# Kernel optimization log

Measured on AMD Instinct MI355X. Metric: run time of the kernel, lower is better.

Reference implementation:

```python
import jax, jax.numpy as jnp
import numpy as np

# Blade order: 1 | e0 e1 e2 e3 | e01 e02 e03 e12 e13 e23 | e012 e013 e023 e123 | e0123
GRADE = jnp.array([0, 1, 1, 1, 1, 2, 2, 2, 2, 2, 2, 3, 3, 3, 3, 4])
# Invariant bilinear form <~A B>_0 for signature (+,-,-,-)
METRIC = jnp.array([1., 1., -1., -1., -1., -1., -1., -1., 1., 1., 1., 1., 1., 1., -1., -1.], dtype=jnp.float32)
NUM_HEADS, HID_MV, HID_S = 8, 8, 32


def equi_linear(mv, s, w_mv, w_s2mv, w_mv2s, w_s, b_mv, b_s):
    """Pin(1,3)-equivariant linear layer: grade-projection basis maps + scalar<->grade-0 mixing."""
    w16 = w_mv[:, :, GRADE]  # (out_mv, in_mv, 16): one weight per grade, broadcast over blades
    out_mv = jnp.einsum('oix,...ix->...ox', w16, mv)
    out_mv = out_mv.at[..., 0].add(jnp.einsum('oi,...i->...o', w_s2mv, s) + b_mv)
    out_s = (jnp.einsum('oi,...i->...o', w_s, s)
             + jnp.einsum('oi,...i->...o', w_mv2s, mv[..., 0]) + b_s)
    return out_mv, out_s


def setup_inputs() -> dict:
    key = jax.random.key(0)
    ks = jax.random.split(key, 20)
    B, Nq, Nkv = 4, 2048, 2048
    H, Cm, Cs = NUM_HEADS, HID_MV, HID_S

    def w(k, shape, fan_in):
        return jax.random.normal(k, shape, jnp.float32) / np.sqrt(fan_in).astype(np.float32)

    return {
        'multivectors_kv': jax.random.normal(ks[0], (B, Nkv, 16, 16), jnp.float32),
        'multivectors_q': jax.random.normal(ks[1], (B, Nq, 16, 16), jnp.float32),
        'scalars_kv': jax.random.normal(ks[2], (B, Nkv, 64), jnp.float32),
        'scalars_q': jax.random.normal(ks[3], (B, Nq, 64), jnp.float32),
        # q_linear: 16 mv -> Cm*H=64 mv, 64 s -> Cs*H=256 s
        'wq_mv': w(ks[4], (Cm * H, 16, 5), 16), 'wq_s2mv': w(ks[5], (Cm * H, 64), 64),
        'wq_mv2s': w(ks[6], (Cs * H, 16), 16), 'wq_s': w(ks[7], (Cs * H, 64), 64),
        'bq_mv': jnp.zeros((Cm * H,), jnp.float32), 'bq_s': jnp.zeros((Cs * H,), jnp.float32),
        # kv_linear: 16 mv -> 2*Cm=16 mv, 64 s -> 2*Cs=64 s (multi-query: shared across heads)
        'wkv_mv': w(ks[8], (2 * Cm, 16, 5), 16), 'wkv_s2mv': w(ks[9], (2 * Cm, 64), 64),
        'wkv_mv2s': w(ks[10], (2 * Cs, 16), 16), 'wkv_s': w(ks[11], (2 * Cs, 64), 64),
        'bkv_mv': jnp.zeros((2 * Cm,), jnp.float32), 'bkv_s': jnp.zeros((2 * Cs,), jnp.float32),
        # out_linear: Cm*H=64 mv -> 16 mv, Cs*H=256 s -> 64 s
        'wo_mv': w(ks[12], (16, Cm * H, 5), Cm * H), 'wo_s2mv': w(ks[13], (16, Cs * H), Cs * H),
        'wo_mv2s': w(ks[14], (64, Cm * H), Cm * H), 'wo_s': w(ks[15], (64, Cs * H), Cs * H),
        'bo_mv': jnp.zeros((16,), jnp.float32), 'bo_s': jnp.zeros((64,), jnp.float32),
        'head_scale': jnp.ones((H,), jnp.float32),
    }


def reference(multivectors_kv, multivectors_q, scalars_kv, scalars_q,
              wq_mv, wq_s2mv, wq_mv2s, wq_s, bq_mv, bq_s,
              wkv_mv, wkv_s2mv, wkv_mv2s, wkv_s, bkv_mv, bkv_s,
              wo_mv, wo_s2mv, wo_mv2s, wo_s, bo_mv, bo_s, head_scale):
    B, Nq = multivectors_q.shape[0], multivectors_q.shape[1]
    H, Cm, Cs = NUM_HEADS, HID_MV, HID_S

    q_mv, q_s = equi_linear(multivectors_q, scalars_q, wq_mv, wq_s2mv, wq_mv2s, wq_s, bq_mv, bq_s)
    kv_mv, kv_s = equi_linear(multivectors_kv, scalars_kv, wkv_mv, wkv_s2mv, wkv_mv2s, wkv_s, bkv_mv, bkv_s)
    k_mv, v_mv = jnp.split(kv_mv, 2, axis=-2)  # (B,Nkv,Cm,16) each
    k_s, v_s = jnp.split(kv_s, 2, axis=-1)     # (B,Nkv,Cs) each

    # einops '(hidden num_heads)': hidden is the outer factor
    q_mv = jnp.moveaxis(q_mv.reshape(B, Nq, Cm, H, 16), 3, 1)  # (B,H,Nq,Cm,16)
    q_s = jnp.moveaxis(q_s.reshape(B, Nq, Cs, H), 3, 1)        # (B,H,Nq,Cs)

    scale = np.float32(1.0 / np.sqrt(16 * Cm + Cs))  # flattened feature dim
    scores = (jnp.einsum('bhqcx,bkcx->bhqk', q_mv, k_mv * METRIC)
              + jnp.einsum('bhqs,bks->bhqk', q_s, k_s)) * scale
    attn = jax.nn.softmax(scores, axis=-1)  # (B,H,Nq,Nkv)
    h_mv = jnp.einsum('bhqk,bkcx->bhqcx', attn, v_mv)
    h_s = jnp.einsum('bhqk,bks->bhqs', attn, v_s)

    h_mv = h_mv * head_scale[None, :, None, None, None]
    h_s = h_s * head_scale[None, :, None, None]

    # '(n_heads hidden_channels)': heads outer
    h_mv = jnp.moveaxis(h_mv, 1, 2).reshape(B, Nq, H * Cm, 16)
    h_s = jnp.moveaxis(h_s, 1, 2).reshape(B, Nq, H * Cs)

    return equi_linear(h_mv, h_s, wo_mv, wo_s2mv, wo_mv2s, wo_s, bo_mv, bo_s)
```

## Files before the change

### kernel.cpp

```cpp
#include <hip/hip_runtime.h>
#include <hip/hip_bf16.h>
#include <cstdint>

#define H_  8
#define B_  4
#define NQ  2048
#define NKV 2048
#define DF  160

typedef __attribute__((ext_vector_type(8))) short bf16x8;
typedef __attribute__((ext_vector_type(4))) float f32x4;

__constant__ int   c_grade[16]  = {0,1,1,1,1,2,2,2,2,2,2,3,3,3,3,4};
__constant__ float c_metric[16] = {1.f,1.f,-1.f,-1.f,-1.f,-1.f,-1.f,-1.f,
                                   1.f,1.f,1.f,1.f,1.f,1.f,-1.f,-1.f};

#define SCALE_LOG2E 0.11405506f

__device__ __forceinline__ unsigned short f2bf(float f) {
    union { float f; unsigned u; } v; v.f = f;
    return (unsigned short)((v.u + 0x7FFFu + ((v.u >> 16) & 1u)) >> 16);
}
__device__ __forceinline__ float bf2f(unsigned short u) {
    union { unsigned u; float f; } v; v.u = ((unsigned)u) << 16;
    return v.f;
}

__global__ __launch_bounds__(256) void qproj_kernel(
    const float* __restrict__ mvq,
    const float* __restrict__ sq,
    const float* __restrict__ w_mv,
    const float* __restrict__ w_s2mv,
    const float* __restrict__ w_mv2s,
    const float* __restrict__ w_s,
    const float* __restrict__ b_mv,
    const float* __restrict__ b_s,
    unsigned short* __restrict__ Qbuf)
{
    const int tok0 = blockIdx.x * 16;
    const int b = tok0 / NQ, n0 = tok0 % NQ;
    const int t = threadIdx.x;

    __shared__ float mv_t[256][20];
    __shared__ float s_t[64][20];
    __shared__ float smadd[64][20];

    #pragma unroll
    for (int k = 0; k < 16; ++k)
        mv_t[t][k] = mvq[(size_t)(tok0 + k) * 256 + t];
    {
        int e = t & 63, tb = t >> 6;
        #pragma unroll
        for (int k = 0; k < 4; ++k)
            s_t[e][tb + 4 * k] = sq[(size_t)(tok0 + tb + 4 * k) * 64 + e];
    }
    __syncthreads();

    {
        int o = t >> 2, tg = t & 3;
        f32x4 acc = {0.f, 0.f, 0.f, 0.f};
        for (int i = 0; i < 64; ++i)
            acc += w_s2mv[o * 64 + i] * *(const f32x4*)&s_t[i][tg * 4];
        acc += b_mv[o];
        *(f32x4*)&smadd[o][tg * 4] = acc;
    }
    __syncthreads();

    const int x = t & 15;
    const int g = c_grade[x];
    #pragma unroll
    for (int p = 0; p < 4; ++p) {
        int o = (t >> 4) + 16 * p;
        f32x4 acc[4] = {{0,0,0,0},{0,0,0,0},{0,0,0,0},{0,0,0,0}};
        #pragma unroll
        for (int i = 0; i < 16; ++i) {
            float w = w_mv[(o * 16 + i) * 5 + g];
            #pragma unroll
            for (int k = 0; k < 4; ++k)
                acc[k] += w * *(const f32x4*)&mv_t[i * 16 + x][k * 4];
        }
        if (x == 0) {
            #pragma unroll
            for (int k = 0; k < 4; ++k)
                acc[k] += *(const f32x4*)&smadd[o][k * 4];
        }
        int c = o >> 3, h = o & 7;
        #pragma unroll
        for (int k = 0; k < 4; ++k)
            #pragma unroll
            for (int j = 0; j < 4; ++j)
                Qbuf[((size_t)(b * H_ + h) * NQ + n0 + k * 4 + j) * DF + c * 16 + x] =
                    f2bf(acc[k][j] * SCALE_LOG2E);
    }

    {
        f32x4 acc[4] = {{0,0,0,0},{0,0,0,0},{0,0,0,0},{0,0,0,0}};
        const float4* ws4 = (const float4*)w_s;
        #pragma unroll
        for (int ii = 0; ii < 16; ++ii) {
            float4 w4 = ws4[t * 16 + ii];
            #pragma unroll
            for (int c = 0; c < 4; ++c) {
                float w = (&w4.x)[c];
                #pragma unroll
                for (int k = 0; k < 4; ++k)
                    acc[k] += w * *(const f32x4*)&s_t[ii * 4 + c][k * 4];
            }
        }
        #pragma unroll
        for (int i = 0; i < 16; ++i) {
            float w = w_mv2s[t * 16 + i];
            #pragma unroll
            for (int k = 0; k < 4; ++k)
                acc[k] += w * *(const f32x4*)&mv_t[i * 16][k * 4];
        }
        float bs = b_s[t];
        int cs = t >> 3, h = t & 7;
        #pragma unroll
        for (int k = 0; k < 4; ++k)
            #pragma unroll
            for (int j = 0; j < 4; ++j)
                Qbuf[((size_t)(b * H_ + h) * NQ + n0 + k * 4 + j) * DF + 128 + cs] =
                    f2bf((acc[k][j] + bs) * SCALE_LOG2E);
    }
}

__global__ __launch_bounds__(256) void kvproj_kernel(
    const float* __restrict__ mvkv, const float* __restrict__ skv,
    const float* __restrict__ w_mv,
    const float* __restrict__ w_s2mv,
    const float* __restrict__ w_mv2s,
    const float* __restrict__ w_s,
    const float* __restrict__ b_mv,
    const float* __restrict__ b_s,
    unsigned short* __restrict__ Kbuf,
    unsigned short* __restrict__ Vtbuf)
{
    const int tok0 = blockIdx.x * 16;
    const int b = tok0 / NKV, n0 = tok0 % NKV;
    const int t = threadIdx.x;

    __shared__ float mv_t[256][20];
    __shared__ float s_t[64][20];
    __shared__ float smadd[16][20];

    #pragma unroll
    for (int k = 0; k < 16; ++k)
        mv_t[t][k] = mvkv[(size_t)(tok0 + k) * 256 + t];
    {
        int e = t & 63, tb = t >> 6;
        #pragma unroll
        for (int k = 0; k < 4; ++k)
            s_t[e][tb + 4 * k] = skv[(size_t)(tok0 + tb + 4 * k) * 64 + e];
    }
    __syncthreads();

    {
        int o = t >> 4, tau = t & 15;
        float acc = 0.f;
        for (int i = 0; i < 64; ++i)
            acc += w_s2mv[o * 64 + i] * s_t[i][tau];
        smadd[o][tau] = acc + b_mv[o];
    }
    __syncthreads();

    {
        int o = t >> 4, x = t & 15, g = c_grade[x];
        f32x4 acc[4] = {{0,0,0,0},{0,0,0,0},{0,0,0,0},{0,0,0,0}};
        #pragma unroll
        for (int i = 0; i < 16; ++i) {
            float w = w_mv[(o * 16 + i) * 5 + g];
            #pragma unroll
            for (int k = 0; k < 4; ++k)
                acc[k] += w * *(const f32x4*)&mv_t[i * 16 + x][k * 4];
        }
        if (x == 0) {
            #pragma unroll
            for (int k = 0; k < 4; ++k)
                acc[k] += *(const f32x4*)&smadd[o][k * 4];
        }
        if (o < 8) {
            float met = c_metric[x];
            #pragma unroll
            for (int k = 0; k < 4; ++k)
                #pragma unroll
                for (int j = 0; j < 4; ++j)
                    Kbuf[((size_t)b * NKV + n0 + k * 4 + j) * DF + o * 16 + x] =
                        f2bf(acc[k][j] * met);
        } else {
            uint4 pk[2];
            unsigned* pu = (unsigned*)&pk[0];
            #pragma unroll
            for (int q = 0; q < 8; ++q) {
                int k = q >> 1, j = (q & 1) * 2;
                pu[q] = (unsigned)f2bf(acc[k][j]) | ((unsigned)f2bf(acc[k][j + 1]) << 16);
            }
            unsigned short* dst = Vtbuf + ((size_t)b * DF + (o - 8) * 16 + x) * NKV + n0;
            ((uint4*)dst)[0] = pk[0];
            ((uint4*)dst)[1] = pk[1];
        }
    }

    {
        int o2 = t & 63, tg = t >> 6;
        f32x4 acc = {0.f, 0.f, 0.f, 0.f};
        const float4* ws4 = (const float4*)w_s;
        #pragma unroll
        for (int ii = 0; ii < 16; ++ii) {
            float4 w4 = ws4[o2 * 16 + ii];
            #pragma unroll
            for (int c = 0; c < 4; ++c)
                acc += (&w4.x)[c] * *(const f32x4*)&s_t[ii * 4 + c][tg * 4];
        }
        #pragma unroll
        for (int i = 0; i < 16; ++i)
            acc += w_mv2s[o2 * 16 + i] * *(const f32x4*)&mv_t[i * 16][tg * 4];
        acc += b_s[o2];
        if (o2 < 32) {
            #pragma unroll
            for (int j = 0; j < 4; ++j)
                Kbuf[((size_t)b * NKV + n0 + tg * 4 + j) * DF + 128 + o2] = f2bf(acc[j]);
        } else {
            uint2 pk;
            pk.x = (unsigned)f2bf(acc[0]) | ((unsigned)f2bf(acc[1]) << 16);
            pk.y = (unsigned)f2bf(acc[2]) | ((unsigned)f2bf(acc[3]) << 16);
            *(uint2*)(Vtbuf + ((size_t)b * DF + 128 + o2 - 32) * NKV + n0 + tg * 4) = pk;
        }
    }
}

__global__ __launch_bounds__(256) void attn_kernel(
    const unsigned short* __restrict__ Qb,
    const unsigned short* __restrict__ Kb0,
    const unsigned short* __restrict__ Vb0,
    const float* __restrict__ head_scale,
    unsigned short* __restrict__ Hb)
{
    const int qt = blockIdx.x, h = blockIdx.y, b = blockIdx.z;
    const int tid  = threadIdx.x;
    const int w    = tid >> 6;
    const int lane = tid & 63;
    const int l16  = lane & 15;
    const int lq   = lane >> 4;
    const int qbase = qt * 64;

    __shared__ __align__(16) unsigned short Ksh[64][168];
    __shared__ __align__(16) unsigned short Vsh[176][72];
    __shared__ __align__(16) unsigned short Psh[4][16][72];

    #pragma unroll
    for (int p = 0; p < 4; ++p) {
        int idx = tid + 256 * p;
        Vsh[160 + (idx >> 6)][idx & 63] = 0x3F80;
    }

    bf16x8 qf[5];
    {
        const unsigned short* qrow =
            Qb + ((size_t)(b * H_ + h) * NQ + qbase + w * 16 + l16) * DF;
        #pragma unroll
        for (int ks = 0; ks < 5; ++ks)
            qf[ks] = *reinterpret_cast<const bf16x8*>(qrow + ks * 32 + lq * 8);
    }

    f32x4 O[11];
    #pragma unroll
    for (int d = 0; d < 11; ++d) O[d] = f32x4{0.f, 0.f, 0.f, 0.f};

    const unsigned short* Kb = Kb0 + (size_t)b * NKV * DF;
    const unsigned short* Vb = Vb0 + (size_t)b * DF * NKV;

    for (int kt = 0; kt < NKV / 64; ++kt) {
        __syncthreads();
        #pragma unroll
        for (int c = 0; c < 5; ++c) {
            int idx = tid + c * 256;
            int r = idx / 20, col = idx % 20;
            *reinterpret_cast<uint4*>(&Ksh[r][col * 8]) =
                *reinterpret_cast<const uint4*>(Kb + (size_t)(kt * 64 + r) * DF + col * 8);
        }
        #pragma unroll
        for (int c = 0; c < 5; ++c) {
            int idx = tid + c * 256;
            int r = idx >> 3, col = idx & 7;
            *reinterpret_cast<uint4*>(&Vsh[r][col * 8]) =
                *reinterpret_cast<const uint4*>(Vb + (size_t)r * NKV + kt * 64 + col * 8);
        }
        __syncthreads();

        f32x4 sc[4];
        #pragma unroll
        for (int nt = 0; nt < 4; ++nt) {
            f32x4 a = f32x4{0.f, 0.f, 0.f, 0.f};
            #pragma unroll
            for (int ks = 0; ks < 5; ++ks) {
                bf16x8 kf = *reinterpret_cast<const bf16x8*>(
                    &Ksh[nt * 16 + l16][ks * 32 + lq * 8]);
                a = __builtin_amdgcn_mfma_f32_16x16x32_bf16(qf[ks], kf, a, 0, 0, 0);
            }
            sc[nt] = a;
        }

        #pragma unroll
        for (int nt = 0; nt < 4; ++nt)
            #pragma unroll
            for (int r = 0; r < 4; ++r)
                Psh[w][lq * 4 + r][nt * 16 + l16] =
                    f2bf(__builtin_amdgcn_exp2f(sc[nt][r]));

        #pragma unroll
        for (int k2 = 0; k2 < 2; ++k2) {
            bf16x8 pf = *reinterpret_cast<const bf16x8*>(
                &Psh[w][l16][k2 * 32 + lq * 8]);
            #pragma unroll
            for (int d = 0; d < 11; ++d) {
                bf16x8 vf = *reinterpret_cast<const bf16x8*>(
                    &Vsh[d * 16 + l16][k2 * 32 + lq * 8]);
                O[d] = __builtin_amdgcn_mfma_f32_16x16x32_bf16(pf, vf, O[d], 0, 0, 0);
            }
        }
    }

    float hsc = head_scale[h];
    #pragma unroll
    for (int r = 0; r < 4; ++r) {
        float inv = hsc / O[10][r];
        int qrow = qbase + w * 16 + lq * 4 + r;
        unsigned short* orow = Hb + ((size_t)(b * H_ + h) * NQ + qrow) * DF;
        #pragma unroll
        for (int d = 0; d < 10; ++d)
            orow[d * 16 + l16] = f2bf(O[d][r] * inv);
    }
}

__global__ __launch_bounds__(256) void oproj_kernel(
    const unsigned short* __restrict__ Hb,
    const float* __restrict__ w_mv,
    const float* __restrict__ w_s2mv,
    const float* __restrict__ w_mv2s,
    const float* __restrict__ w_s,
    const float* __restrict__ b_mv,
    const float* __restrict__ b_s,
    float* __restrict__ out)
{
    const int tok0 = blockIdx.x * 8;
    const int b = tok0 / NQ, n0 = tok0 % NQ;
    const int t = threadIdx.x;

    __shared__ float hmv_t[1024][12];
    __shared__ float hs_t[256][12];
    __shared__ float s2v[16][8];

    #pragma unroll
    for (int hh = 0; hh < 8; ++hh) {
        #pragma unroll
        for (int j = 0; j < 5; ++j) {
            int flat = t + 256 * j;
            int tau = flat / 160, d = flat % 160;
            float v = bf2f(Hb[((size_t)(b * H_ + hh) * NQ + n0 + tau) * DF + d]);
            if (d < 128) hmv_t[hh * 128 + d][tau] = v;
            else         hs_t[hh * 32 + d - 128][tau] = v;
        }
    }
    __syncthreads();

    {
        int o2 = t >> 4, tau = (t >> 1) & 7, ih = t & 1;
        float acc = 0.f;
        for (int ii = 0; ii < 128; ++ii) {
            int i = ih * 128 + ii;
            acc += w_s2mv[o2 * 256 + i] * hs_t[i][tau];
        }
        acc += __shfl_xor(acc, 1);
        if (ih == 0) s2v[o2][tau] = acc + b_mv[o2];
    }
    __syncthreads();

    {
        int o2 = t >> 4, x = t & 15, g = c_grade[x];
        f32x4 a0 = {0,0,0,0}, a1 = {0,0,0,0};
        for (int i = 0; i < 64; ++i) {
            float w = w_mv[(o2 * 64 + i) * 5 + g];
            a0 += w * *(const f32x4*)&hmv_t[i * 16 + x][0];
            a1 += w * *(const f32x4*)&hmv_t[i * 16 + x][4];
        }
        if (x == 0) {
            a0 += *(const f32x4*)&s2v[o2][0];
            a1 += *(const f32x4*)&s2v[o2][4];
        }
        #pragma unroll
        for (int j = 0; j < 4; ++j) {
            out[(size_t)(tok0 + j) * 256 + o2 * 16 + x] = a0[j];
            out[(size_t)(tok0 + 4 + j) * 256 + o2 * 16 + x] = a1[j];
        }
    }

    {
        int o2 = t & 63, th = t >> 6;
        float a0 = b_s[o2], a1 = b_s[o2];
        const float4* ws4 = (const float4*)w_s;
        for (int ii = 0; ii < 64; ++ii) {
            float4 w4 = ws4[o2 * 64 + ii];
            #pragma unroll
            for (int c = 0; c < 4; ++c) {
                int i = ii * 4 + c;
                float w = (&w4.x)[c];
                a0 += w * hs_t[i][th * 2];
                a1 += w * hs_t[i][th * 2 + 1];
            }
        }
        for (int i = 0; i < 64; ++i) {
            float w = w_mv2s[o2 * 64 + i];
            a0 += w * hmv_t[i * 16][th * 2];
            a1 += w * hmv_t[i * 16][th * 2 + 1];
        }
        size_t sbase = (size_t)B_ * NQ * 256;
        out[sbase + (size_t)(tok0 + th * 2) * 64 + o2] = a0;
        out[sbase + (size_t)(tok0 + th * 2 + 1) * 64 + o2] = a1;
    }
}

extern "C" void kernel_launch(void* const* d_in, const int* in_sizes, int n_in,
                              void* d_out, int out_size, void* d_ws, size_t ws_size,
                              hipStream_t stream) {
    const float* mv_kv  = (const float*)d_in[0];
    const float* mv_q   = (const float*)d_in[1];
    const float* s_kv   = (const float*)d_in[2];
    const float* s_q    = (const float*)d_in[3];
    const float* wq_mv  = (const float*)d_in[4];
    const float* wq_s2mv= (const float*)d_in[5];
    const float* wq_mv2s= (const float*)d_in[6];
    const float* wq_s   = (const float*)d_in[7];
    const float* bq_mv  = (const float*)d_in[8];
    const float* bq_s   = (const float*)d_in[9];
    const float* wkv_mv = (const float*)d_in[10];
    const float* wkv_s2mv=(const float*)d_in[11];
    const float* wkv_mv2s=(const float*)d_in[12];
    const float* wkv_s  = (const float*)d_in[13];
    const float* bkv_mv = (const float*)d_in[14];
    const float* bkv_s  = (const float*)d_in[15];
    const float* wo_mv  = (const float*)d_in[16];
    const float* wo_s2mv= (const float*)d_in[17];
    const float* wo_mv2s= (const float*)d_in[18];
    const float* wo_s   = (const float*)d_in[19];
    const float* bo_mv  = (const float*)d_in[20];
    const float* bo_s   = (const float*)d_in[21];
    const float* head_scale = (const float*)d_in[22];

    char* ws = (char*)d_ws;
    unsigned short* Qbuf  = (unsigned short*)(ws);
    unsigned short* Kbuf  = (unsigned short*)(ws + 20971520);
    unsigned short* Vtbuf = (unsigned short*)(ws + 23592960);
    unsigned short* Hbuf  = (unsigned short*)(ws + 26214400);

    qproj_kernel<<<B_ * NQ / 16, 256, 0, stream>>>(
        mv_q, s_q, wq_mv, wq_s2mv, wq_mv2s, wq_s, bq_mv, bq_s, Qbuf);
    kvproj_kernel<<<B_ * NKV / 16, 256, 0, stream>>>(
        mv_kv, s_kv, wkv_mv, wkv_s2mv, wkv_mv2s, wkv_s, bkv_mv, bkv_s, Kbuf, Vtbuf);
    dim3 g3(NQ / 64, H_, B_);
    attn_kernel<<<g3, 256, 0, stream>>>(Qbuf, Kbuf, Vtbuf, head_scale, Hbuf);
    oproj_kernel<<<B_ * NQ / 8, 256, 0, stream>>>(
        Hbuf, wo_mv, wo_s2mv, wo_mv2s, wo_s, bo_mv, bo_s, (float*)d_out);
}
```

Measured before the change: 343.8 us.

## Process two heads per attention block to reuse K/V tiles; restructure Q projection

The attention kernel now handles two heads per workgroup, sharing each loaded K and V tile in LDS across both heads' MFMA chains, which halves the global K/V traffic and the tile-load syncs. The row-sum column is now computed by MFMA against an in-register vector of ones instead of a padded LDS row. The Q projection also caches weights in registers and reuses the loaded mv rows across four outputs. The cost is higher register pressure (two sets of accumulators, with launch bounds asking for two blocks per CU) and half as many attention blocks.

```diff
diff --git a/kernel.cpp b/kernel.cpp
--- a/kernel.cpp
+++ b/kernel.cpp
@@ -68,29 +68,37 @@
 
     const int x = t & 15;
     const int g = c_grade[x];
-    #pragma unroll
-    for (int p = 0; p < 4; ++p) {
-        int o = (t >> 4) + 16 * p;
-        f32x4 acc[4] = {{0,0,0,0},{0,0,0,0},{0,0,0,0},{0,0,0,0}};
-        #pragma unroll
-        for (int i = 0; i < 16; ++i) {
-            float w = w_mv[(o * 16 + i) * 5 + g];
-            #pragma unroll
-            for (int k = 0; k < 4; ++k)
-                acc[k] += w * *(const f32x4*)&mv_t[i * 16 + x][k * 4];
-        }
-        if (x == 0) {
-            #pragma unroll
-            for (int k = 0; k < 4; ++k)
-                acc[k] += *(const f32x4*)&smadd[o][k * 4];
-        }
-        int c = o >> 3, h = o & 7;
-        #pragma unroll
-        for (int k = 0; k < 4; ++k)
-            #pragma unroll
-            for (int j = 0; j < 4; ++j)
-                Qbuf[((size_t)(b * H_ + h) * NQ + n0 + k * 4 + j) * DF + c * 16 + x] =
-                    f2bf(acc[k][j] * SCALE_LOG2E);
+    const int obase = t >> 4;
+    {
+        float wreg[4][16];
+        #pragma unroll
+        for (int p = 0; p < 4; ++p) {
+            int o = obase + 16 * p;
+            #pragma unroll
+            for (int i = 0; i < 16; ++i)
+                wreg[p][i] = w_mv[(o * 16 + i) * 5 + g];
+        }
+        #pragma unroll
+        for (int k = 0; k < 4; ++k) {
+            f32x4 rows[16];
+            #pragma unroll
+            for (int i = 0; i < 16; ++i)
+                rows[i] = *(const f32x4*)&mv_t[i * 16 + x][k * 4];
+            #pragma unroll
+            for (int p = 0; p < 4; ++p) {
+                int o = obase + 16 * p;
+                f32x4 acc = {0.f, 0.f, 0.f, 0.f};
+                #pragma unroll
+                for (int i = 0; i < 16; ++i)
+                    acc += wreg[p][i] * rows[i];
+                if (x == 0) acc += *(const f32x4*)&smadd[o][k * 4];
+                int c = o >> 3, h = o & 7;
+                #pragma unroll
+                for (int j = 0; j < 4; ++j)
+                    Qbuf[((size_t)(b * H_ + h) * NQ + n0 + k * 4 + j) * DF + c * 16 + x] =
+                        f2bf(acc[j] * SCALE_LOG2E);
+            }
+        }
     }
 
     {
@@ -229,14 +237,14 @@
     }
 }
 
-__global__ __launch_bounds__(256) void attn_kernel(
+__global__ __launch_bounds__(256, 2) void attn_kernel(
     const unsigned short* __restrict__ Qb,
     const unsigned short* __restrict__ Kb0,
     const unsigned short* __restrict__ Vb0,
     const float* __restrict__ head_scale,
     unsigned short* __restrict__ Hb)
 {
-    const int qt = blockIdx.x, h = blockIdx.y, b = blockIdx.z;
+    const int qt = blockIdx.x, hp = blockIdx.y, b = blockIdx.z;
     const int tid  = threadIdx.x;
     const int w    = tid >> 6;
     const int lane = tid & 63;
@@ -245,27 +253,28 @@
     const int qbase = qt * 64;
 
     __shared__ __align__(16) unsigned short Ksh[64][168];
-    __shared__ __align__(16) unsigned short Vsh[176][72];
-    __shared__ __align__(16) unsigned short Psh[4][16][72];
-
-    #pragma unroll
-    for (int p = 0; p < 4; ++p) {
-        int idx = tid + 256 * p;
-        Vsh[160 + (idx >> 6)][idx & 63] = 0x3F80;
-    }
-
-    bf16x8 qf[5];
-    {
+    __shared__ __align__(16) unsigned short Vsh[160][72];
+    __shared__ __align__(16) unsigned short Psh[2][4][16][72];
+
+    bf16x8 onesf;
+    #pragma unroll
+    for (int j = 0; j < 8; ++j) onesf[j] = (short)0x3F80;
+
+    bf16x8 qf[2][5];
+    #pragma unroll
+    for (int s = 0; s < 2; ++s) {
         const unsigned short* qrow =
-            Qb + ((size_t)(b * H_ + h) * NQ + qbase + w * 16 + l16) * DF;
+            Qb + ((size_t)(b * H_ + hp * 2 + s) * NQ + qbase + w * 16 + l16) * DF;
         #pragma unroll
         for (int ks = 0; ks < 5; ++ks)
-            qf[ks] = *reinterpret_cast<const bf16x8*>(qrow + ks * 32 + lq * 8);
-    }
-
-    f32x4 O[11];
-    #pragma unroll
-    for (int d = 0; d < 11; ++d) O[d] = f32x4{0.f, 0.f, 0.f, 0.f};
+            qf[s][ks] = *reinterpret_cast<const bf16x8*>(qrow + ks * 32 + lq * 8);
+    }
+
+    f32x4 O[2][11];
+    #pragma unroll
+    for (int s = 0; s < 2; ++s)
+        #pragma unroll
+        for (int d = 0; d < 11; ++d) O[s][d] = f32x4{0.f, 0.f, 0.f, 0.f};
 
     const unsigned short* Kb = Kb0 + (size_t)b * NKV * DF;
     const unsigned short* Vb = Vb0 + (size_t)b * DF * NKV;
@@ -288,48 +297,58 @@
         }
         __syncthreads();
 
-        f32x4 sc[4];
+        f32x4 sc[2][4];
         #pragma unroll
         for (int nt = 0; nt < 4; ++nt) {
-            f32x4 a = f32x4{0.f, 0.f, 0.f, 0.f};
+            sc[0][nt] = f32x4{0.f, 0.f, 0.f, 0.f};
+            sc[1][nt] = f32x4{0.f, 0.f, 0.f, 0.f};
             #pragma unroll
             for (int ks = 0; ks < 5; ++ks) {
                 bf16x8 kf = *reinterpret_cast<const bf16x8*>(
                     &Ksh[nt * 16 + l16][ks * 32 + lq * 8]);
-                a = __builtin_amdgcn_mfma_f32_16x16x32_bf16(qf[ks], kf, a, 0, 0, 0);
-            }
-            sc[nt] = a;
-        }
-
-        #pragma unroll
-        for (int nt = 0; nt < 4; ++nt)
-            #pragma unroll
-            for (int r = 0; r < 4; ++r)
-                Psh[w][lq * 4 + r][nt * 16 + l16] =
-                    f2bf(__builtin_amdgcn_exp2f(sc[nt][r]));
+                sc[0][nt] = __builtin_amdgcn_mfma_f32_16x16x32_bf16(qf[0][ks], kf, sc[0][nt], 0, 0, 0);
+                sc[1][nt] = __builtin_amdgcn_mfma_f32_16x16x32_bf16(qf[1][ks], kf, sc[1][nt], 0, 0, 0);
+            }
+        }
+
+        #pragma unroll
+        for (int s = 0; s < 2; ++s)
+            #pragma unroll
+            for (int nt = 0; nt < 4; ++nt)
+                #pragma unroll
+                for (int r = 0; r < 4; ++r)
+                    Psh[s][w][lq * 4 + r][nt * 16 + l16] =
+                        f2bf(__builtin_amdgcn_exp2f(sc[s][nt][r]));
 
         #pragma unroll
         for (int k2 = 0; k2 < 2; ++k2) {
-            bf16x8 pf = *reinterpret_cast<const bf16x8*>(
-                &Psh[w][l16][k2 * 32 + lq * 8]);
-            #pragma unroll
-            for (int d = 0; d < 11; ++d) {
+            bf16x8 pf0 = *reinterpret_cast<const bf16x8*>(&Psh[0][w][l16][k2 * 32 + lq * 8]);
+            bf16x8 pf1 = *reinterpret_cast<const bf16x8*>(&Psh[1][w][l16][k2 * 32 + lq * 8]);
+            O[0][10] = __builtin_amdgcn_mfma_f32_16x16x32_bf16(pf0, onesf, O[0][10], 0, 0, 0);
+            O[1][10] = __builtin_amdgcn_mfma_f32_16x16x32_bf16(pf1, onesf, O[1][10], 0, 0, 0);
+            #pragma unroll
+            for (int d = 0; d < 10; ++d) {
                 bf16x8 vf = *reinterpret_cast<const bf16x8*>(
                     &Vsh[d * 16 + l16][k2 * 32 + lq * 8]);
-                O[d] = __builtin_amdgcn_mfma_f32_16x16x32_bf16(pf, vf, O[d], 0, 0, 0);
-            }
-        }
-    }
-
-    float hsc = head_scale[h];
-    #pragma unroll
-    for (int r = 0; r < 4; ++r) {
-        float inv = hsc / O[10][r];
-        int qrow = qbase + w * 16 + lq * 4 + r;
-        unsigned short* orow = Hb + ((size_t)(b * H_ + h) * NQ + qrow) * DF;
-        #pragma unroll
-        for (int d = 0; d < 10; ++d)
-            orow[d * 16 + l16] = f2bf(O[d][r] * inv);
+                O[0][d] = __builtin_amdgcn_mfma_f32_16x16x32_bf16(pf0, vf, O[0][d], 0, 0, 0);
+                O[1][d] = __builtin_amdgcn_mfma_f32_16x16x32_bf16(pf1, vf, O[1][d], 0, 0, 0);
+            }
+        }
+    }
+
+    #pragma unroll
+    for (int s = 0; s < 2; ++s) {
+        float hsc = head_scale[hp * 2 + s];
+        #pragma unroll
+        for (int r = 0; r < 4; ++r) {
+            float inv = hsc / O[s][10][r];
+            int qrow = qbase + w * 16 + lq * 4 + r;
+            unsigned short* orow =
+                Hb + ((size_t)(b * H_ + hp * 2 + s) * NQ + qrow) * DF;
+            #pragma unroll
+            for (int d = 0; d < 10; ++d)
+                orow[d * 16 + l16] = f2bf(O[s][d][r] * inv);
+        }
     }
 }
 
@@ -457,7 +476,7 @@
         mv_q, s_q, wq_mv, wq_s2mv, wq_mv2s, wq_s, bq_mv, bq_s, Qbuf);
     kvproj_kernel<<<B_ * NKV / 16, 256, 0, stream>>>(
         mv_kv, s_kv, wkv_mv, wkv_s2mv, wkv_mv2s, wkv_s, bkv_mv, bkv_s, Kbuf, Vtbuf);
-    dim3 g3(NQ / 64, H_, B_);
+    dim3 g3(NQ / 64, H_ / 2, B_);
     attn_kernel<<<g3, 256, 0, stream>>>(Qbuf, Kbuf, Vtbuf, head_scale, Hbuf);
     oproj_kernel<<<B_ * NQ / 8, 256, 0, stream>>>(
         Hbuf, wo_mv, wo_s2mv, wo_mv2s, wo_s, bo_mv, bo_s, (float*)d_out);
```

After: 290.4 us. 15.5% less time.
